# Optimization experiments

Hardware: AMD Instinct MI355X
Metric: run time of the kernel (lower is better)

The kernel has to match this reference:

```python
import jax, jax.numpy as jnp
import numpy as np

EPS = 1e-6

def _ln(x, g, b):
    m = x.mean(-1, keepdims=True)
    v = jnp.var(x, axis=-1, keepdims=True)
    return (x - m) * jax.lax.rsqrt(v + EPS) * g + b

def _mha(x, qkv_w, out_w, out_b, heads, dh):
    # vit-style attention: Linear(dim, 3*heads*dh, bias=False), chunk into q,k,v
    B, N, _ = x.shape
    qkv = (x @ qkv_w).reshape(B, N, 3, heads, dh).transpose(2, 0, 3, 1, 4)
    q, k, v = qkv[0], qkv[1], qkv[2]                       # [B,H,N,dh]
    attn = jax.nn.softmax(jnp.einsum('bhid,bhjd->bhij', q, k) * (dh ** -0.5), axis=-1)
    o = jnp.einsum('bhij,bhjd->bhid', attn, v).transpose(0, 2, 1, 3).reshape(B, N, heads * dh)
    return o @ out_w + out_b

def _tx(x, p, heads, dh):
    # standard prenorm transformer stack, p = stacked per-layer params
    (l1g, l1b, qw, ow, ob, l2g, l2b, f1w, f1b, f2w, f2b, ng, nb) = p
    for i in range(l1g.shape[0]):
        x = x + _mha(_ln(x, l1g[i], l1b[i]), qw[i], ow[i], ob[i], heads, dh)
        h = _ln(x, l2g[i], l2b[i])
        x = x + jax.nn.gelu(h @ f1w[i] + f1b[i]) @ f2w[i] + f2b[i]
    return _ln(x, ng, nb)

def _ats(x, l1g, l1b, qkvw, qkvb, projw, projb, l2g, l2b, f1w, f1b, f2w, f2b):
    # ATS block: attention + CLS-significance-driven adaptive token resampling (gather)
    B, N, D = x.shape
    heads = 6
    dh = D // heads
    h = _ln(x, l1g, l1b)
    qkv = (h @ qkvw + qkvb).reshape(B, N, 3, heads, dh).transpose(2, 0, 3, 1, 4)
    q, k, v = qkv[0], qkv[1], qkv[2]
    attn = jax.nn.softmax(jnp.einsum('bhid,bhjd->bhij', q, k) * (dh ** -0.5), axis=-1)  # [B,H,N,N]
    y = jnp.einsum('bhij,bhjd->bhid', attn, v).transpose(0, 2, 1, 3).reshape(B, N, D)
    y = y @ projw + projb
    # significance score: cls attention * value norm (ATS, Fayyaz et al.)
    vn = jnp.linalg.norm(v, axis=-1)                        # [B,H,N]
    s = (attn[:, :, 0, 1:] * vn[:, :, 1:]).mean(axis=1)     # [B,N-1]
    s = s / (s.sum(-1, keepdims=True) + 1e-8)
    cdf = jnp.cumsum(s, axis=-1)                            # [B,N-1]
    # deterministic inverse-transform sampling of N-1 tokens
    u = (jnp.arange(N - 1, dtype=x.dtype) + 0.5) / (N - 1)
    idx = jax.vmap(lambda c: jnp.searchsorted(c, u))(cdf)
    idx = jnp.clip(idx, 0, N - 2) + 1                       # skip cls slot
    idx = jnp.concatenate([jnp.zeros((B, 1), idx.dtype), idx], axis=1)  # keep cls
    g = lambda a: jnp.take_along_axis(a, idx[:, :, None], axis=1)
    x = g(x) + g(y)
    h = _ln(x, l2g, l2b)
    return x + jax.nn.gelu(h @ f1w + f1b) @ f2w + f2b

def reference(x, patch_w, patch_b, pos_emb, space_token, temporal_token,
              s_ln1_g, s_ln1_b, s_qkv_w, s_out_w, s_out_b, s_ln2_g, s_ln2_b,
              s_fc1_w, s_fc1_b, s_fc2_w, s_fc2_b, s_norm_g, s_norm_b,
              t_ln1_g, t_ln1_b, t_qkv_w, t_out_w, t_out_b, t_ln2_g, t_ln2_b,
              t_fc1_w, t_fc1_b, t_fc2_w, t_fc2_b, t_norm_g, t_norm_b,
              a_ln1_g, a_ln1_b, a_qkv_w, a_qkv_b, a_proj_w, a_proj_b,
              a_ln2_g, a_ln2_b, a_fc1_w, a_fc1_b, a_fc2_w, a_fc2_b,
              final_g, final_b, h1_w, h1_b, h2_w, h2_b):
    B, T = x.shape[0], x.shape[1]
    BT, D, P, HP = B * T, 192, 16, 14
    # patch embedding (conv16s16 as unfold + linear), channel-major flattening
    xt = x.reshape(BT, 3, HP, P, HP, P).transpose(0, 2, 4, 1, 3, 5).reshape(BT, HP * HP, 3 * P * P)
    xt = (xt @ patch_w + patch_b).reshape(B, T, HP * HP, D)
    cls = jnp.broadcast_to(space_token.reshape(1, 1, 1, D), (B, T, 1, D))
    xt = jnp.concatenate([cls, xt], axis=2) + pos_emb      # [B,T,197,D]
    xt = xt.reshape(BT, 197, D)
    xt = _tx(xt, (s_ln1_g, s_ln1_b, s_qkv_w, s_out_w, s_out_b, s_ln2_g, s_ln2_b,
                  s_fc1_w, s_fc1_b, s_fc2_w, s_fc2_b, s_norm_g, s_norm_b), 6, 64)
    for i in range(a_ln1_g.shape[0]):
        xt = _ats(xt, a_ln1_g[i], a_ln1_b[i], a_qkv_w[i], a_qkv_b[i], a_proj_w[i],
                  a_proj_b[i], a_ln2_g[i], a_ln2_b[i], a_fc1_w[i], a_fc1_b[i],
                  a_fc2_w[i], a_fc2_b[i])
    xc = xt[:, 0].reshape(B, T, D)
    tt = jnp.broadcast_to(temporal_token, (B, 1, D))
    xc = jnp.concatenate([tt, xc], axis=1)                 # [B,T+1,D]
    xc = _tx(xc, (t_ln1_g, t_ln1_b, t_qkv_w, t_out_w, t_out_b, t_ln2_g, t_ln2_b,
                  t_fc1_w, t_fc1_b, t_fc2_w, t_fc2_b, t_norm_g, t_norm_b), 6, 64)
    f = jnp.max(xc, axis=1)                                # AdaptiveMaxPool1d(1) over tokens
    f = _ln(f, final_g, final_b)
    return jax.nn.relu(f @ h1_w + h1_b) @ h2_w + h2_b      # mlp_head -> [B,2]

def setup_inputs():
    key = jax.random.key(0)
    ks = iter(jax.random.split(key, 64))
    def rn(shape, s=0.02):
        return jax.random.normal(next(ks), shape, dtype=jnp.float32) * s
    d = {}
    d['x'] = jax.random.normal(next(ks), (16, 5, 3, 224, 224), dtype=jnp.float32)
    d['patch_w'] = rn((768, 192)); d['patch_b'] = jnp.zeros((192,), jnp.float32)
    d['pos_emb'] = rn((1, 5, 197, 192))
    d['space_token'] = rn((1, 1, 192)); d['temporal_token'] = rn((1, 1, 192))
    def tx(depth, n):
        d[n + '_ln1_g'] = jnp.ones((depth, 192), jnp.float32); d[n + '_ln1_b'] = jnp.zeros((depth, 192), jnp.float32)
        d[n + '_qkv_w'] = rn((depth, 192, 1152)); d[n + '_out_w'] = rn((depth, 384, 192)); d[n + '_out_b'] = jnp.zeros((depth, 192), jnp.float32)
        d[n + '_ln2_g'] = jnp.ones((depth, 192), jnp.float32); d[n + '_ln2_b'] = jnp.zeros((depth, 192), jnp.float32)
        d[n + '_fc1_w'] = rn((depth, 192, 768)); d[n + '_fc1_b'] = jnp.zeros((depth, 768), jnp.float32)
        d[n + '_fc2_w'] = rn((depth, 768, 192)); d[n + '_fc2_b'] = jnp.zeros((depth, 192), jnp.float32)
        d[n + '_norm_g'] = jnp.ones((192,), jnp.float32); d[n + '_norm_b'] = jnp.zeros((192,), jnp.float32)
    tx(2, 's'); tx(3, 't')
    d['a_ln1_g'] = jnp.ones((12, 192), jnp.float32); d['a_ln1_b'] = jnp.zeros((12, 192), jnp.float32)
    d['a_qkv_w'] = rn((12, 192, 576)); d['a_qkv_b'] = jnp.zeros((12, 576), jnp.float32)
    d['a_proj_w'] = rn((12, 192, 192)); d['a_proj_b'] = jnp.zeros((12, 192), jnp.float32)
    d['a_ln2_g'] = jnp.ones((12, 192), jnp.float32); d['a_ln2_b'] = jnp.zeros((12, 192), jnp.float32)
    d['a_fc1_w'] = rn((12, 192, 768)); d['a_fc1_b'] = jnp.zeros((12, 768), jnp.float32)
    d['a_fc2_w'] = rn((12, 768, 192)); d['a_fc2_b'] = jnp.zeros((12, 192), jnp.float32)
    d['final_g'] = jnp.ones((192,), jnp.float32); d['final_b'] = jnp.zeros((192,), jnp.float32)
    d['h1_w'] = rn((192, 64)); d['h1_b'] = jnp.zeros((64,), jnp.float32)
    d['h2_w'] = rn((64, 2)); d['h2_b'] = jnp.zeros((2,), jnp.float32)
    return d
```

## Files before the change

kernel.cpp:

```cpp
#include <hip/hip_runtime.h>
#include <hip/hip_bf16.h>
#include <math.h>

typedef float in_t;
typedef float out_t;

__device__ __forceinline__ float ldi(const in_t* p, size_t i) { return (float)p[i]; }

#define DMODEL 192
#define NTOK   197
#define BT_    80
#define ROWS_  (BT_*NTOK)

__device__ __forceinline__ float gelu_f(float v) {
  return 0.5f*v*(1.f + tanhf(0.7978845608028654f*(v + 0.044715f*v*v*v)));
}

__device__ __forceinline__ short f2bf(float f) {
  union { float f; unsigned u; } v; v.f = f;
  unsigned r = v.u + 0x7FFFu + ((v.u >> 16) & 1u);
  return (short)(r >> 16);
}

typedef __attribute__((ext_vector_type(8))) short bfrag;
typedef __attribute__((ext_vector_type(4))) float f32x4;

__global__ __launch_bounds__(256)
void wconv_k(const float* __restrict__ W, short* __restrict__ O, int K, int N)
{
  __shared__ float tile[32][33];
  const int l = blockIdx.z;
  const int k0 = blockIdx.y*32, n0 = blockIdx.x*32;
  const float* Wl = W + (size_t)l*K*N;
  short* Ol = O + (size_t)l*K*N;
  const int tx = threadIdx.x & 31, ty = threadIdx.x >> 5;
  #pragma unroll
  for (int r = ty; r < 32; r += 8) {
    int k = k0 + r, n = n0 + tx;
    tile[r][tx] = (k < K && n < N) ? Wl[(size_t)k*N + n] : 0.f;
  }
  __syncthreads();
  #pragma unroll
  for (int r = ty; r < 32; r += 8) {
    int n = n0 + r, k = k0 + tx;
    if (n < N && k < K) Ol[(size_t)n*K + k] = f2bf(tile[tx][r]);
  }
}

template<int EPI>
__global__ __launch_bounds__(256)
void gemmM_k(const float* __restrict__ A, const short* __restrict__ Wt,
             const in_t* __restrict__ bias, const float* __restrict__ R,
             float* __restrict__ C, int M, int N, int K)
{
  constexpr int BM=64, BN=64, BK=32, LP=BK+8;
  __shared__ short Asb[BM][LP];
  __shared__ short Bsb[BN][LP];
  const int t = threadIdx.x;
  const int w = t >> 6, lane = t & 63;
  const int bm0 = blockIdx.y*BM, bn0 = blockIdx.x*BN;
  const int sr = t >> 2;
  const int sk = (t & 3) * 8;
  f32x4 acc[4] = {};

  for (int k0 = 0; k0 < K; k0 += BK) {
    {
      int gm = bm0 + sr;
      short y[8];
      if (gm < M) {
        const float* ap = A + (size_t)gm*K + k0 + sk;
        float4 v0 = *(const float4*)ap;
        float4 v1 = *(const float4*)(ap + 4);
        y[0]=f2bf(v0.x); y[1]=f2bf(v0.y); y[2]=f2bf(v0.z); y[3]=f2bf(v0.w);
        y[4]=f2bf(v1.x); y[5]=f2bf(v1.y); y[6]=f2bf(v1.z); y[7]=f2bf(v1.w);
      } else {
        #pragma unroll
        for (int i=0;i<8;++i) y[i]=0;
      }
      *(bfrag*)&Asb[sr][sk] = *(bfrag*)y;
      bfrag bv = *(const bfrag*)(Wt + (size_t)(bn0 + sr)*K + k0 + sk);
      *(bfrag*)&Bsb[sr][sk] = bv;
    }
    __syncthreads();
    const int fr = lane & 15, kg = (lane >> 4) * 8;
    bfrag af = *(const bfrag*)&Asb[w*16 + fr][kg];
    #pragma unroll
    for (int nt = 0; nt < 4; ++nt) {
      bfrag bf = *(const bfrag*)&Bsb[nt*16 + fr][kg];
      acc[nt] = __builtin_amdgcn_mfma_f32_16x16x32_bf16(af, bf, acc[nt], 0, 0, 0);
    }
    __syncthreads();
  }
  const int col = lane & 15, rg = (lane >> 4) * 4;
  #pragma unroll
  for (int nt = 0; nt < 4; ++nt) {
    int gn = bn0 + nt*16 + col;
    float bv = bias ? ldi(bias, gn) : 0.f;
    #pragma unroll
    for (int r = 0; r < 4; ++r) {
      int gm = bm0 + w*16 + rg + r;
      if (gm < M) {
        float v = acc[nt][r] + bv;
        if (EPI==1) v = gelu_f(v);
        if (EPI==2) v += R[(size_t)gm*N + gn];
        C[(size_t)gm*N + gn] = v;
      }
    }
  }
}

__global__ __launch_bounds__(256)
void ln_k(const float* __restrict__ x, const in_t* __restrict__ g, const in_t* __restrict__ b,
          float* __restrict__ o, int rows)
{
  int t = threadIdx.x, wave = t>>6, lane = t&63;
  int r = blockIdx.x*4 + wave;
  if (r >= rows) return;
  const float* xr = x + (size_t)r*DMODEL;
  float e0 = xr[lane], e1 = xr[lane+64], e2 = xr[lane+128];
  float s = e0+e1+e2;
  #pragma unroll
  for (int off=32; off; off>>=1) s += __shfl_xor(s, off);
  float mean = s / 192.f;
  float d0=e0-mean, d1=e1-mean, d2=e2-mean;
  float v = d0*d0+d1*d1+d2*d2;
  #pragma unroll
  for (int off=32; off; off>>=1) v += __shfl_xor(v, off);
  float rs = 1.f / sqrtf(v/192.f + 1e-6f);
  float* orow = o + (size_t)r*DMODEL;
  orow[lane]     = d0*rs*ldi(g,lane)     + ldi(b,lane);
  orow[lane+64]  = d1*rs*ldi(g,lane+64)  + ldi(b,lane+64);
  orow[lane+128] = d2*rs*ldi(g,lane+128) + ldi(b,lane+128);
}

template<int DH, int W>
__global__ __launch_bounds__(W*64)
void attnM_k(const float* __restrict__ qkv, float* __restrict__ out,
             float* __restrict__ attn0, int heads, float scale)
{
  constexpr int NSEQ = 197;
  constexpr int NP   = 224;
  constexpr int KG   = DH/8;
  constexpr int CT   = DH/16;
  constexpr int NF   = DH/32;
  __shared__ short Kb[KG][NP][8];
  __shared__ short Vt[NP/8][DH][8];
  __shared__ short Ps[W][NP/8][16][8];

  const int bh = blockIdx.x;
  const int b = bh / heads, h = bh - b*heads;
  const int stride = 3*heads*DH;
  const float* __restrict__ base = qkv + (size_t)b*NSEQ*stride;
  const int qo = h*DH, ko = heads*DH + h*DH, vo = 2*heads*DH + h*DH;
  const int t = threadIdx.x, w = t>>6, lane = t&63;

  for (int idx = t; idx < NP*DH; idx += W*64) {
    int j = idx / DH, d = idx - j*DH;
    float kv = 0.f, vv = 0.f;
    if (j < NSEQ) {
      kv = base[(size_t)j*stride + ko + d];
      vv = base[(size_t)j*stride + vo + d];
    }
    Kb[d>>3][j][d&7] = f2bf(kv);
    Vt[j>>3][d][j&7] = f2bf(vv);
  }
  __syncthreads();

  const int c = lane & 15, g = lane >> 4, rg = g*4;
  const float NEG = -3.0e38f;

  for (int st = w; st < 13; st += W) {
    const int q0 = st*16;
    int qrow = q0 + c; if (qrow > NSEQ-1) qrow = NSEQ-1;
    bfrag aq[NF];
    {
      const float* qp = base + (size_t)qrow*stride + qo + g*8;
      #pragma unroll
      for (int f = 0; f < NF; ++f) {
        float4 v0 = *(const float4*)(qp + f*32);
        float4 v1 = *(const float4*)(qp + f*32 + 4);
        short y[8] = {f2bf(v0.x),f2bf(v0.y),f2bf(v0.z),f2bf(v0.w),
                      f2bf(v1.x),f2bf(v1.y),f2bf(v1.z),f2bf(v1.w)};
        aq[f] = *(bfrag*)y;
      }
    }
    f32x4 sacc[14];
    #pragma unroll
    for (int jt = 0; jt < 14; ++jt) sacc[jt] = (f32x4){0.f,0.f,0.f,0.f};
    #pragma unroll
    for (int jt = 0; jt < 13; ++jt) {
      #pragma unroll
      for (int f = 0; f < NF; ++f) {
        bfrag bk = *(const bfrag*)&Kb[f*4 + g][jt*16 + c][0];
        sacc[jt] = __builtin_amdgcn_mfma_f32_16x16x32_bf16(aq[f], bk, sacc[jt], 0, 0, 0);
      }
    }
    float m0[4] = {NEG,NEG,NEG,NEG};
    #pragma unroll
    for (int jt = 0; jt < 14; ++jt) {
      const bool valid = (jt < 13) && (jt*16 + c < NSEQ);
      #pragma unroll
      for (int r = 0; r < 4; ++r) {
        float sv = valid ? sacc[jt][r]*scale : NEG;
        sacc[jt][r] = sv;
        m0[r] = fmaxf(m0[r], sv);
      }
    }
    #pragma unroll
    for (int off = 1; off < 16; off <<= 1)
      #pragma unroll
      for (int r = 0; r < 4; ++r) m0[r] = fmaxf(m0[r], __shfl_xor(m0[r], off));
    float sum[4] = {0.f,0.f,0.f,0.f};
    #pragma unroll
    for (int jt = 0; jt < 14; ++jt)
      #pragma unroll
      for (int r = 0; r < 4; ++r) {
        float e = expf(sacc[jt][r] - m0[r]);
        sacc[jt][r] = e;
        sum[r] += e;
      }
    #pragma unroll
    for (int off = 1; off < 16; off <<= 1)
      #pragma unroll
      for (int r = 0; r < 4; ++r) sum[r] += __shfl_xor(sum[r], off);
    float inv[4];
    #pragma unroll
    for (int r = 0; r < 4; ++r) inv[r] = 1.f / sum[r];

    if (attn0 != nullptr && st == 0 && g == 0) {
      #pragma unroll
      for (int jt = 0; jt < 13; ++jt) {
        int j = jt*16 + c;
        if (j < NSEQ) attn0[(size_t)bh*NSEQ + j] = sacc[jt][0]*inv[0];
      }
    }
    #pragma unroll
    for (int jt = 0; jt < 14; ++jt)
      #pragma unroll
      for (int r = 0; r < 4; ++r)
        Ps[w][jt*2 + (c>>3)][rg + r][c&7] = f2bf(sacc[jt][r]);
    f32x4 oacc[CT];
    #pragma unroll
    for (int ct = 0; ct < CT; ++ct) oacc[ct] = (f32x4){0.f,0.f,0.f,0.f};
    #pragma unroll
    for (int kc = 0; kc < 7; ++kc) {
      bfrag ap = *(const bfrag*)&Ps[w][kc*4 + g][c][0];
      #pragma unroll
      for (int ct = 0; ct < CT; ++ct) {
        bfrag bv = *(const bfrag*)&Vt[kc*4 + g][ct*16 + c][0];
        oacc[ct] = __builtin_amdgcn_mfma_f32_16x16x32_bf16(ap, bv, oacc[ct], 0, 0, 0);
      }
    }
    #pragma unroll
    for (int ct = 0; ct < CT; ++ct)
      #pragma unroll
      for (int r = 0; r < 4; ++r) {
        int q = q0 + rg + r;
        if (q < NSEQ)
          out[((size_t)b*NSEQ + q)*(size_t)(heads*DH) + h*DH + ct*16 + c] = oacc[ct][r]*inv[r];
      }
  }
}

template<int DH, int W>
__global__ __launch_bounds__(W*64)
void attn2r_k(const float* __restrict__ qkv, float* __restrict__ out,
              float* __restrict__ attn0, int Nseq, int heads, float scale)
{
  constexpr int QT = 8;
  constexpr int KTS = 204;
  constexpr int NPART = (DH == 64) ? 1 : 2;
  constexpr int DQ   = DH/4;
  constexpr int QPG  = 2;
  __shared__ float Kt[DH * KTS];
  __shared__ float Qt[W][DH][12];
  __shared__ float Ps[W][QT][200];

  const int bh = blockIdx.x;
  const int b = bh / heads, h = bh % heads;
  const int stride = 3 * heads * DH;
  const float* __restrict__ base = qkv + (size_t)b * Nseq * stride;
  const int qo = h * DH, ko = heads * DH + h * DH, vo = 2 * heads * DH + h * DH;
  const int t = threadIdx.x, w = t >> 6, lane = t & 63;

  for (int idx = t; idx < Nseq * DH; idx += W * 64) {
    int j = idx / DH, d0 = idx - j * DH;
    Kt[d0 * KTS + j] = base[(size_t)j * stride + ko + d0];
  }
  __syncthreads();

  const int d = lane & (DH - 1);
  const int nchunks = (Nseq + QT - 1) / QT;
  const int jcmax = (Nseq + 3) >> 2;
  const float NEG = -3.0e38f;
  const float4* Kt4 = (const float4*)Kt;

  const int part = (NPART == 2) ? (lane >> 5) : 0;
  const int qg   = (DH == 64) ? (lane >> 4) : ((lane >> 3) & 3);
  const int dq   = lane & (DQ - 1);
  const int dv   = 4 * dq;

  for (int ic = w; ic < nchunks; ic += W) {
    const int i0 = ic * QT;
    if ((DH == 64) || (lane >> 5) == 0) {
      #pragma unroll
      for (int q = 0; q < QT; ++q) {
        int i = i0 + q;
        Qt[w][d][q] = (i < Nseq) ? base[(size_t)i * stride + qo + d] : 0.f;
      }
    }
    float s[QT][4];
    #pragma unroll
    for (int q = 0; q < QT; ++q)
      #pragma unroll
      for (int u = 0; u < 4; ++u) s[q][u] = 0.f;
    #pragma unroll 4
    for (int dd = 0; dd < DH; ++dd) {
      float4 kv = (lane < 51) ? Kt4[dd * (KTS/4) + lane] : make_float4(0.f,0.f,0.f,0.f);
      float4 qA = *(const float4*)&Qt[w][dd][0];
      float4 qB = *(const float4*)&Qt[w][dd][4];
      float qv[8] = {qA.x, qA.y, qA.z, qA.w, qB.x, qB.y, qB.z, qB.w};
      float kr[4] = {kv.x, kv.y, kv.z, kv.w};
      #pragma unroll
      for (int q = 0; q < QT; ++q)
        #pragma unroll
        for (int u = 0; u < 4; ++u)
          s[q][u] = fmaf(qv[q], kr[u], s[q][u]);
    }
    float inv[QT];
    #pragma unroll
    for (int q = 0; q < QT; ++q) {
      float mx = NEG;
      #pragma unroll
      for (int u = 0; u < 4; ++u) {
        int j = 4*lane + u;
        s[q][u] = (j < Nseq) ? s[q][u]*scale : NEG;
        mx = fmaxf(mx, s[q][u]);
      }
      #pragma unroll
      for (int off = 32; off; off >>= 1) mx = fmaxf(mx, __shfl_xor(mx, off));
      float sum = 0.f;
      #pragma unroll
      for (int u = 0; u < 4; ++u) {
        float p = (4*lane + u < Nseq) ? expf(s[q][u] - mx) : 0.f;
        s[q][u] = p; sum += p;
      }
      #pragma unroll
      for (int off = 32; off; off >>= 1) sum += __shfl_xor(sum, off);
      inv[q] = 1.f / sum;
      if (lane < 50)
        *(float4*)&Ps[w][q][4*lane] = make_float4(s[q][0], s[q][1], s[q][2], s[q][3]);
    }
    if (attn0 != nullptr && i0 == 0) {
      #pragma unroll
      for (int u = 0; u < 4; ++u) {
        int j = 4*lane + u;
        if (j < Nseq) attn0[(size_t)bh*Nseq + j] = s[0][u]*inv[0];
      }
    }
    float o[QPG][4];
    #pragma unroll
    for (int qi = 0; qi < QPG; ++qi) { o[qi][0]=0.f; o[qi][1]=0.f; o[qi][2]=0.f; o[qi][3]=0.f; }
    const float* __restrict__ Vg = base + vo;
    for (int jc = part; jc < jcmax; jc += NPART) {
      const int jb = 4*jc;
      float4 V0 = make_float4(0.f,0.f,0.f,0.f), V1=V0, V2=V0, V3=V0;
      if (jb+0 < Nseq) V0 = *(const float4*)&Vg[(size_t)(jb+0)*stride + dv];
      if (jb+1 < Nseq) V1 = *(const float4*)&Vg[(size_t)(jb+1)*stride + dv];
      if (jb+2 < Nseq) V2 = *(const float4*)&Vg[(size_t)(jb+2)*stride + dv];
      if (jb+3 < Nseq) V3 = *(const float4*)&Vg[(size_t)(jb+3)*stride + dv];
      #pragma unroll
      for (int qi = 0; qi < QPG; ++qi) {
        float4 p4 = *(const float4*)&Ps[w][qg*QPG+qi][jb];
        o[qi][0] = fmaf(p4.w,V3.x, fmaf(p4.z,V2.x, fmaf(p4.y,V1.x, fmaf(p4.x,V0.x, o[qi][0]))));
        o[qi][1] = fmaf(p4.w,V3.y, fmaf(p4.z,V2.y, fmaf(p4.y,V1.y, fmaf(p4.x,V0.y, o[qi][1]))));
        o[qi][2] = fmaf(p4.w,V3.z, fmaf(p4.z,V2.z, fmaf(p4.y,V1.z, fmaf(p4.x,V0.z, o[qi][2]))));
        o[qi][3] = fmaf(p4.w,V3.w, fmaf(p4.z,V2.w, fmaf(p4.y,V1.w, fmaf(p4.x,V0.w, o[qi][3]))));
      }
    }
    if (NPART == 2) {
      #pragma unroll
      for (int qi = 0; qi < QPG; ++qi) {
        o[qi][0] += __shfl_xor(o[qi][0], 32);
        o[qi][1] += __shfl_xor(o[qi][1], 32);
        o[qi][2] += __shfl_xor(o[qi][2], 32);
        o[qi][3] += __shfl_xor(o[qi][3], 32);
      }
    }
    if (part == 0) {
      #pragma unroll
      for (int qi = 0; qi < QPG; ++qi) {
        float iv = inv[qi];
        if (qg == 1) iv = inv[QPG + qi];
        if (qg == 2) iv = inv[2*QPG + qi];
        if (qg == 3) iv = inv[3*QPG + qi];
        int i = i0 + qg*QPG + qi;
        if (i < Nseq) {
          float4 r = make_float4(o[qi][0]*iv, o[qi][1]*iv, o[qi][2]*iv, o[qi][3]*iv);
          *(float4*)&out[((size_t)b*Nseq + i)*(size_t)(heads*DH) + h*DH + dv] = r;
        }
      }
    }
  }
}

__global__ void patchify_k(const in_t* __restrict__ x, float* __restrict__ A)
{
  int idx = blockIdx.x*256 + threadIdx.x;
  const int total = BT_*196*768;
  if (idx >= total) return;
  int kc = idx % 768;
  int m  = idx / 768;
  int p  = m % 196;
  int bt = m / 196;
  int c  = kc >> 8;
  int py = (kc >> 4) & 15;
  int px = kc & 15;
  int ph = p / 14, pw = p % 14;
  size_t src = (((size_t)bt*3 + c)*224 + (ph*16+py))*224 + (pw*16+px);
  A[idx] = ldi(x, src);
}

__global__ void assemble_k(const float* __restrict__ pt, const in_t* __restrict__ st,
                           const in_t* __restrict__ pe, float* __restrict__ X)
{
  int i = blockIdx.x*256 + threadIdx.x;
  const int total = BT_*NTOK*DMODEL;
  if (i >= total) return;
  int d  = i % DMODEL;
  int n  = (i / DMODEL) % NTOK;
  int bt = i / (DMODEL*NTOK);
  int tt = bt % 5;
  float base = (n == 0) ? ldi(st, d)
                        : pt[((size_t)bt*196 + (n-1))*DMODEL + d];
  X[i] = base + ldi(pe, ((size_t)tt*NTOK + n)*DMODEL + d);
}

__global__ void score_k(const float* __restrict__ attn0, const float* __restrict__ qkv,
                        float* __restrict__ S)
{
  int b = blockIdx.x;
  int jj = threadIdx.x;
  if (jj >= 196) return;
  int j = jj + 1;
  float acc = 0.f;
  #pragma unroll
  for (int h = 0; h < 6; ++h) {
    float a0 = attn0[((size_t)b*6 + h)*NTOK + j];
    const float* v = qkv + ((size_t)b*NTOK + j)*576 + 384 + h*32;
    float ss = 0.f;
    #pragma unroll
    for (int d = 0; d < 32; ++d) ss += v[d]*v[d];
    acc += a0 * sqrtf(ss);
  }
  S[(size_t)b*196 + jj] = acc / 6.0f;
}

__global__ void sample_k(const float* __restrict__ S, int* __restrict__ idxout)
{
  __shared__ float cdf[196];
  int b = blockIdx.x, t = threadIdx.x;
  if (t == 0) {
    float tot = 0.f;
    for (int k = 0; k < 196; ++k) tot += S[(size_t)b*196 + k];
    float denom = tot + 1e-8f;
    float run = 0.f;
    for (int k = 0; k < 196; ++k) { run += S[(size_t)b*196 + k] / denom; cdf[k] = run; }
    idxout[(size_t)b*NTOK] = 0;
  }
  __syncthreads();
  if (t < 196) {
    float u = ((float)t + 0.5f) / 196.0f;
    int cnt = 0;
    for (int k = 0; k < 196; ++k) cnt += (cdf[k] < u) ? 1 : 0;
    int c = cnt > 195 ? 195 : cnt;
    idxout[(size_t)b*NTOK + 1 + t] = c + 1;
  }
}

__global__ void gather_k(const float* __restrict__ X, const float* __restrict__ P,
                         const int* __restrict__ idx, float* __restrict__ Xo)
{
  int i = blockIdx.x*256 + threadIdx.x;
  const int total = BT_*NTOK*DMODEL;
  if (i >= total) return;
  int d  = i % DMODEL;
  int n  = (i / DMODEL) % NTOK;
  int bt = i / (DMODEL*NTOK);
  int src = idx[(size_t)bt*NTOK + n];
  size_t sr = ((size_t)bt*NTOK + src)*DMODEL + d;
  Xo[i] = X[sr] + P[sr];
}

__global__ void build_xc_k(const float* __restrict__ X, const in_t* __restrict__ tt,
                           float* __restrict__ xc)
{
  int i = blockIdx.x*256 + threadIdx.x;
  const int total = 16*6*DMODEL;
  if (i >= total) return;
  int d = i % DMODEL;
  int n = (i / DMODEL) % 6;
  int b = i / (DMODEL*6);
  xc[i] = (n == 0) ? ldi(tt, d)
                   : X[(((size_t)b*5 + (n-1))*NTOK + 0)*DMODEL + d];
}

__global__ __launch_bounds__(256)
void head_k(const float* __restrict__ xc, const in_t* __restrict__ fg, const in_t* __restrict__ fb,
            const in_t* __restrict__ w1, const in_t* __restrict__ b1,
            const in_t* __restrict__ w2, const in_t* __restrict__ b2,
            out_t* __restrict__ outp)
{
  __shared__ float fn[DMODEL];
  __shared__ float hid[64];
  __shared__ float mv[2];
  int b = blockIdx.x, t = threadIdx.x;
  if (t < DMODEL) {
    float m = xc[((size_t)b*6 + 0)*DMODEL + t];
    #pragma unroll
    for (int n = 1; n < 6; ++n) m = fmaxf(m, xc[((size_t)b*6 + n)*DMODEL + t]);
    fn[t] = m;
  }
  __syncthreads();
  if (t == 0) {
    float s = 0.f;
    for (int d = 0; d < DMODEL; ++d) s += fn[d];
    float mean = s / 192.f;
    float v = 0.f;
    for (int d = 0; d < DMODEL; ++d) { float dd = fn[d]-mean; v += dd*dd; }
    mv[0] = mean; mv[1] = 1.f / sqrtf(v/192.f + 1e-6f);
  }
  __syncthreads();
  if (t < DMODEL) fn[t] = (fn[t]-mv[0])*mv[1]*ldi(fg,t) + ldi(fb,t);
  __syncthreads();
  if (t < 64) {
    float a = ldi(b1, t);
    for (int d = 0; d < DMODEL; ++d) a += fn[d]*ldi(w1, (size_t)d*64 + t);
    hid[t] = fmaxf(a, 0.f);
  }
  __syncthreads();
  if (t < 2) {
    float a = ldi(b2, t);
    for (int j = 0; j < 64; ++j) a += hid[j]*ldi(w2, (size_t)j*2 + t);
    outp[(size_t)b*2 + t] = (out_t)a;
  }
}

extern "C" void kernel_launch(void* const* d_in, const int* in_sizes, int n_in,
                              void* d_out, int out_size, void* d_ws, size_t ws_size,
                              hipStream_t stream)
{
  if (n_in < 50) return;
  const in_t* x_in     = (const in_t*)d_in[0];
  const in_t* patch_w  = (const in_t*)d_in[1];
  const in_t* patch_b  = (const in_t*)d_in[2];
  const in_t* pos_emb  = (const in_t*)d_in[3];
  const in_t* space_tk = (const in_t*)d_in[4];
  const in_t* temp_tk  = (const in_t*)d_in[5];
  const in_t* s_ln1_g = (const in_t*)d_in[6];  const in_t* s_ln1_b = (const in_t*)d_in[7];
  const in_t* s_qkv_w = (const in_t*)d_in[8];  const in_t* s_out_w = (const in_t*)d_in[9];
  const in_t* s_out_b = (const in_t*)d_in[10]; const in_t* s_ln2_g = (const in_t*)d_in[11];
  const in_t* s_ln2_b = (const in_t*)d_in[12]; const in_t* s_fc1_w = (const in_t*)d_in[13];
  const in_t* s_fc1_b = (const in_t*)d_in[14]; const in_t* s_fc2_w = (const in_t*)d_in[15];
  const in_t* s_fc2_b = (const in_t*)d_in[16]; const in_t* s_nrm_g = (const in_t*)d_in[17];
  const in_t* s_nrm_b = (const in_t*)d_in[18];
  const in_t* t_ln1_g = (const in_t*)d_in[19]; const in_t* t_ln1_b = (const in_t*)d_in[20];
  const in_t* t_qkv_w = (const in_t*)d_in[21]; const in_t* t_out_w = (const in_t*)d_in[22];
  const in_t* t_out_b = (const in_t*)d_in[23]; const in_t* t_ln2_g = (const in_t*)d_in[24];
  const in_t* t_ln2_b = (const in_t*)d_in[25]; const in_t* t_fc1_w = (const in_t*)d_in[26];
  const in_t* t_fc1_b = (const in_t*)d_in[27]; const in_t* t_fc2_w = (const in_t*)d_in[28];
  const in_t* t_fc2_b = (const in_t*)d_in[29]; const in_t* t_nrm_g = (const in_t*)d_in[30];
  const in_t* t_nrm_b = (const in_t*)d_in[31];
  const in_t* a_ln1_g = (const in_t*)d_in[32]; const in_t* a_ln1_b = (const in_t*)d_in[33];
  const in_t* a_qkv_w = (const in_t*)d_in[34]; const in_t* a_qkv_b = (const in_t*)d_in[35];
  const in_t* a_prj_w = (const in_t*)d_in[36]; const in_t* a_prj_b = (const in_t*)d_in[37];
  const in_t* a_ln2_g = (const in_t*)d_in[38]; const in_t* a_ln2_b = (const in_t*)d_in[39];
  const in_t* a_fc1_w = (const in_t*)d_in[40]; const in_t* a_fc1_b = (const in_t*)d_in[41];
  const in_t* a_fc2_w = (const in_t*)d_in[42]; const in_t* a_fc2_b = (const in_t*)d_in[43];
  const in_t* final_g = (const in_t*)d_in[44]; const in_t* final_b = (const in_t*)d_in[45];
  const in_t* h1_w = (const in_t*)d_in[46];    const in_t* h1_b = (const in_t*)d_in[47];
  const in_t* h2_w = (const in_t*)d_in[48];    const in_t* h2_b = (const in_t*)d_in[49];

  float* ws = (float*)d_ws;
  size_t off = 0;
  auto alloc = [&](size_t nf) { size_t r = off; off += (nf + 63) & ~((size_t)63); return r; };
  size_t oX   = alloc((size_t)ROWS_*DMODEL);
  size_t oX2  = alloc((size_t)ROWS_*DMODEL);
  size_t oH   = alloc((size_t)ROWS_*DMODEL);
  size_t oQKV = alloc((size_t)ROWS_*1152);
  size_t oY   = alloc((size_t)ROWS_*384);
  size_t oFF  = alloc((size_t)ROWS_*768);
  size_t oA0  = alloc((size_t)480*NTOK);
  size_t oSB  = alloc((size_t)BT_*196);
  size_t oXC  = alloc((size_t)16*6*DMODEL);
  size_t oIDX = alloc((size_t)BT_*NTOK);
  size_t oWB  = alloc((size_t)4202496 + 64);
  if (ws_size < off*sizeof(float)) return;

  float* X   = ws + oX;
  float* X2  = ws + oX2;
  float* H   = ws + oH;
  float* QKV = ws + oQKV;
  float* Y   = ws + oY;
  float* FF  = ws + oFF;
  float* A0  = ws + oA0;
  float* SB  = ws + oSB;
  float* XC  = ws + oXC;
  int*   IDX = (int*)(ws + oIDX);
  short* WB  = (short*)(ws + oWB);

  size_t wo = 0;
  auto wslot = [&](size_t n){ size_t r = wo; wo += n; return r; };
  size_t wPatch = wslot(147456);
  size_t wSqkv  = wslot(442368);
  size_t wSout  = wslot(147456);
  size_t wSfc1  = wslot(294912);
  size_t wSfc2  = wslot(294912);
  size_t wAqkv  = wslot(1327104);
  size_t wAprj  = wslot(442368);
  size_t wAfc1  = wslot(1769472);
  size_t wAfc2  = wslot(1769472);
  size_t wTqkv  = wslot(663552);
  size_t wTout  = wslot(221184);
  size_t wTfc1  = wslot(442368);
  size_t wTfc2  = wslot(442368);

  auto wconv = [&](const in_t* W, size_t slot, int K, int N, int L) {
    dim3 g(N/32, K/32, L);
    hipLaunchKernelGGL(wconv_k, g, dim3(256), 0, stream, W, WB + slot, K, N);
  };
  wconv(patch_w, wPatch, 768, 192, 1);
  wconv(s_qkv_w, wSqkv, 192, 1152, 2);
  wconv(s_out_w, wSout, 384, 192, 2);
  wconv(s_fc1_w, wSfc1, 192, 768, 2);
  wconv(s_fc2_w, wSfc2, 768, 192, 2);
  wconv(a_qkv_w, wAqkv, 192, 576, 12);
  wconv(a_prj_w, wAprj, 192, 192, 12);
  wconv(a_fc1_w, wAfc1, 192, 768, 12);
  wconv(a_fc2_w, wAfc2, 768, 192, 12);
  wconv(t_qkv_w, wTqkv, 192, 1152, 3);
  wconv(t_out_w, wTout, 384, 192, 3);
  wconv(t_fc1_w, wTfc1, 192, 768, 3);
  wconv(t_fc2_w, wTfc2, 768, 192, 3);

  auto gemm = [&](int epi, const float* A, const short* Wt, const in_t* bias,
                  const float* R, float* C, int M, int N, int K) {
    dim3 grid(N/64, (M+63)/64);
    if (epi == 0)      hipLaunchKernelGGL(gemmM_k<0>, grid, dim3(256), 0, stream, A, Wt, bias, R, C, M, N, K);
    else if (epi == 1) hipLaunchKernelGGL(gemmM_k<1>, grid, dim3(256), 0, stream, A, Wt, bias, R, C, M, N, K);
    else               hipLaunchKernelGGL(gemmM_k<2>, grid, dim3(256), 0, stream, A, Wt, bias, R, C, M, N, K);
  };
  auto ln = [&](const float* xi, const in_t* g, const in_t* b, float* o, int rows) {
    hipLaunchKernelGGL(ln_k, dim3((rows+3)/4), dim3(256), 0, stream, xi, g, b, o, rows);
  };

  {
    int total = BT_*196*768;
    hipLaunchKernelGGL(patchify_k, dim3((total+255)/256), dim3(256), 0, stream, x_in, FF);
    gemm(0, FF, WB + wPatch, patch_b, nullptr, Y, BT_*196, DMODEL, 768);
    int tot2 = BT_*NTOK*DMODEL;
    hipLaunchKernelGGL(assemble_k, dim3((tot2+255)/256), dim3(256), 0, stream, Y, space_tk, pos_emb, X);
  }

  const float sc64 = 0.125f;
  const float sc32 = 0.17677669529663687f;

  for (int i = 0; i < 2; ++i) {
    ln(X, s_ln1_g + (size_t)i*192, s_ln1_b + (size_t)i*192, H, ROWS_);
    gemm(0, H, WB + wSqkv + (size_t)i*192*1152, nullptr, nullptr, QKV, ROWS_, 1152, 192);
    hipLaunchKernelGGL((attnM_k<64,8>), dim3(BT_*6), dim3(512), 0, stream, QKV, Y, (float*)nullptr, 6, sc64);
    gemm(2, Y, WB + wSout + (size_t)i*384*192, s_out_b + (size_t)i*192, X, X, ROWS_, 192, 384);
    ln(X, s_ln2_g + (size_t)i*192, s_ln2_b + (size_t)i*192, H, ROWS_);
    gemm(1, H, WB + wSfc1 + (size_t)i*192*768, s_fc1_b + (size_t)i*768, nullptr, FF, ROWS_, 768, 192);
    gemm(2, FF, WB + wSfc2 + (size_t)i*768*192, s_fc2_b + (size_t)i*192, X, X, ROWS_, 192, 768);
  }
  ln(X, s_nrm_g, s_nrm_b, X, ROWS_);

  float* xa = X; float* xb = X2;
  for (int i = 0; i < 12; ++i) {
    ln(xa, a_ln1_g + (size_t)i*192, a_ln1_b + (size_t)i*192, H, ROWS_);
    gemm(0, H, WB + wAqkv + (size_t)i*192*576, a_qkv_b + (size_t)i*576, nullptr, QKV, ROWS_, 576, 192);
    hipLaunchKernelGGL((attnM_k<32,4>), dim3(BT_*6), dim3(256), 0, stream, QKV, Y, A0, 6, sc32);
    gemm(0, Y, WB + wAprj + (size_t)i*192*192, a_prj_b + (size_t)i*192, nullptr, H, ROWS_, 192, 192);
    hipLaunchKernelGGL(score_k, dim3(BT_), dim3(256), 0, stream, A0, QKV, SB);
    hipLaunchKernelGGL(sample_k, dim3(BT_), dim3(256), 0, stream, SB, IDX);
    {
      int tot = BT_*NTOK*DMODEL;
      hipLaunchKernelGGL(gather_k, dim3((tot+255)/256), dim3(256), 0, stream, xa, H, IDX, xb);
    }
    ln(xb, a_ln2_g + (size_t)i*192, a_ln2_b + (size_t)i*192, H, ROWS_);
    gemm(1, H, WB + wAfc1 + (size_t)i*192*768, a_fc1_b + (size_t)i*768, nullptr, FF, ROWS_, 768, 192);
    gemm(2, FF, WB + wAfc2 + (size_t)i*768*192, a_fc2_b + (size_t)i*192, xb, xb, ROWS_, 192, 768);
    float* tmp = xa; xa = xb; xb = tmp;
  }

  {
    int tot = 16*6*DMODEL;
    hipLaunchKernelGGL(build_xc_k, dim3((tot+255)/256), dim3(256), 0, stream, xa, temp_tk, XC);
  }
  const int MT = 16*6;
  for (int i = 0; i < 3; ++i) {
    ln(XC, t_ln1_g + (size_t)i*192, t_ln1_b + (size_t)i*192, H, MT);
    gemm(0, H, WB + wTqkv + (size_t)i*192*1152, nullptr, nullptr, QKV, MT, 1152, 192);
    hipLaunchKernelGGL((attn2r_k<64,8>), dim3(16*6), dim3(512), 0, stream, QKV, Y, (float*)nullptr, 6, 6, sc64);
    gemm(2, Y, WB + wTout + (size_t)i*384*192, t_out_b + (size_t)i*192, XC, XC, MT, 192, 384);
    ln(XC, t_ln2_g + (size_t)i*192, t_ln2_b + (size_t)i*192, H, MT);
    gemm(1, H, WB + wTfc1 + (size_t)i*192*768, t_fc1_b + (size_t)i*768, nullptr, FF, MT, 768, 192);
    gemm(2, FF, WB + wTfc2 + (size_t)i*768*192, t_fc2_b + (size_t)i*192, XC, XC, MT, 192, 768);
  }
  ln(XC, t_nrm_g, t_nrm_b, XC, MT);

  hipLaunchKernelGGL(head_k, dim3(16), dim3(256), 0, stream, XC, final_g, final_b,
                     h1_w, h1_b, h2_w, h2_b, (out_t*)d_out);
}
```

Measured before the change: 2.853 ms.

## Store GEMM intermediates in bf16 and deepen GEMM K-tile to 192

The GEMM kernel now stages a full 192-wide K chunk in LDS per iteration instead of 32, which cuts the number of barrier-synchronised load/compute rounds. It is also templated on bf16 input and output. Attention outputs, the GELU FFN hidden activations and the patchified input are now written as bf16, so the following GEMMs read half the bytes and skip the fp32-to-bf16 conversion. The larger LDS footprint (about 51 KB per block) may lower occupancy, and every K must now be a multiple of 192.

```diff
diff --git a/kernel.cpp b/kernel.cpp
--- a/kernel.cpp
+++ b/kernel.cpp
@@ -47,47 +47,53 @@
   }
 }
 
-template<int EPI>
+template<int EPI, int ABF, int OBF>
 __global__ __launch_bounds__(256)
-void gemmM_k(const float* __restrict__ A, const short* __restrict__ Wt,
-             const in_t* __restrict__ bias, const float* __restrict__ R,
-             float* __restrict__ C, int M, int N, int K)
-{
-  constexpr int BM=64, BN=64, BK=32, LP=BK+8;
-  __shared__ short Asb[BM][LP];
-  __shared__ short Bsb[BN][LP];
+void gemmW_k(const void* __restrict__ Ain, const short* __restrict__ Wt,
+             const float* __restrict__ bias, const float* __restrict__ R,
+             void* __restrict__ Cout, int M, int N, int K)
+{
+  constexpr int LP = 200;
+  __shared__ short Asb[64][LP];
+  __shared__ short Bsb[64][LP];
   const int t = threadIdx.x;
   const int w = t >> 6, lane = t & 63;
-  const int bm0 = blockIdx.y*BM, bn0 = blockIdx.x*BN;
+  const int bm0 = blockIdx.y*64, bn0 = blockIdx.x*64;
   const int sr = t >> 2;
   const int sk = (t & 3) * 8;
   f32x4 acc[4] = {};
 
-  for (int k0 = 0; k0 < K; k0 += BK) {
-    {
-      int gm = bm0 + sr;
-      short y[8];
+  for (int k0 = 0; k0 < K; k0 += 192) {
+    const int gm = bm0 + sr;
+    #pragma unroll
+    for (int cc = 0; cc < 6; ++cc) {
+      const int kk = cc*32 + sk;
+      short y[8] = {0,0,0,0,0,0,0,0};
       if (gm < M) {
-        const float* ap = A + (size_t)gm*K + k0 + sk;
-        float4 v0 = *(const float4*)ap;
-        float4 v1 = *(const float4*)(ap + 4);
-        y[0]=f2bf(v0.x); y[1]=f2bf(v0.y); y[2]=f2bf(v0.z); y[3]=f2bf(v0.w);
-        y[4]=f2bf(v1.x); y[5]=f2bf(v1.y); y[6]=f2bf(v1.z); y[7]=f2bf(v1.w);
-      } else {
-        #pragma unroll
-        for (int i=0;i<8;++i) y[i]=0;
-      }
-      *(bfrag*)&Asb[sr][sk] = *(bfrag*)y;
-      bfrag bv = *(const bfrag*)(Wt + (size_t)(bn0 + sr)*K + k0 + sk);
-      *(bfrag*)&Bsb[sr][sk] = bv;
+        if (ABF == 0) {
+          const float* ap = (const float*)Ain + (size_t)gm*K + k0 + kk;
+          float4 v0 = *(const float4*)ap;
+          float4 v1 = *(const float4*)(ap + 4);
+          y[0]=f2bf(v0.x); y[1]=f2bf(v0.y); y[2]=f2bf(v0.z); y[3]=f2bf(v0.w);
+          y[4]=f2bf(v1.x); y[5]=f2bf(v1.y); y[6]=f2bf(v1.z); y[7]=f2bf(v1.w);
+        } else {
+          *(bfrag*)y = *(const bfrag*)((const short*)Ain + (size_t)gm*K + k0 + kk);
+        }
+      }
+      *(bfrag*)&Asb[sr][kk] = *(bfrag*)y;
+      bfrag bv = *(const bfrag*)(Wt + (size_t)(bn0 + sr)*K + k0 + kk);
+      *(bfrag*)&Bsb[sr][kk] = bv;
     }
     __syncthreads();
-    const int fr = lane & 15, kg = (lane >> 4) * 8;
-    bfrag af = *(const bfrag*)&Asb[w*16 + fr][kg];
-    #pragma unroll
-    for (int nt = 0; nt < 4; ++nt) {
-      bfrag bf = *(const bfrag*)&Bsb[nt*16 + fr][kg];
-      acc[nt] = __builtin_amdgcn_mfma_f32_16x16x32_bf16(af, bf, acc[nt], 0, 0, 0);
+    const int fr = lane & 15, g8 = (lane >> 4) * 8;
+    #pragma unroll
+    for (int ks = 0; ks < 6; ++ks) {
+      bfrag af = *(const bfrag*)&Asb[w*16 + fr][ks*32 + g8];
+      #pragma unroll
+      for (int nt = 0; nt < 4; ++nt) {
+        bfrag bf = *(const bfrag*)&Bsb[nt*16 + fr][ks*32 + g8];
+        acc[nt] = __builtin_amdgcn_mfma_f32_16x16x32_bf16(af, bf, acc[nt], 0, 0, 0);
+      }
     }
     __syncthreads();
   }
@@ -95,7 +101,7 @@
   #pragma unroll
   for (int nt = 0; nt < 4; ++nt) {
     int gn = bn0 + nt*16 + col;
-    float bv = bias ? ldi(bias, gn) : 0.f;
+    float bv = bias ? bias[gn] : 0.f;
     #pragma unroll
     for (int r = 0; r < 4; ++r) {
       int gm = bm0 + w*16 + rg + r;
@@ -103,7 +109,8 @@
         float v = acc[nt][r] + bv;
         if (EPI==1) v = gelu_f(v);
         if (EPI==2) v += R[(size_t)gm*N + gn];
-        C[(size_t)gm*N + gn] = v;
+        if (OBF) ((short*)Cout)[(size_t)gm*N + gn] = f2bf(v);
+        else     ((float*)Cout)[(size_t)gm*N + gn] = v;
       }
     }
   }
@@ -135,7 +142,7 @@
 
 template<int DH, int W>
 __global__ __launch_bounds__(W*64)
-void attnM_k(const float* __restrict__ qkv, float* __restrict__ out,
+void attnM_k(const float* __restrict__ qkv, short* __restrict__ out,
              float* __restrict__ attn0, int heads, float scale)
 {
   constexpr int NSEQ = 197;
@@ -257,7 +264,7 @@
       for (int r = 0; r < 4; ++r) {
         int q = q0 + rg + r;
         if (q < NSEQ)
-          out[((size_t)b*NSEQ + q)*(size_t)(heads*DH) + h*DH + ct*16 + c] = oacc[ct][r]*inv[r];
+          out[((size_t)b*NSEQ + q)*(size_t)(heads*DH) + h*DH + ct*16 + c] = f2bf(oacc[ct][r]*inv[r]);
       }
   }
 }
@@ -404,7 +411,7 @@
   }
 }
 
-__global__ void patchify_k(const in_t* __restrict__ x, float* __restrict__ A)
+__global__ void patchify_k(const in_t* __restrict__ x, short* __restrict__ A)
 {
   int idx = blockIdx.x*256 + threadIdx.x;
   const int total = BT_*196*768;
@@ -418,7 +425,7 @@
   int px = kc & 15;
   int ph = p / 14, pw = p % 14;
   size_t src = (((size_t)bt*3 + c)*224 + (ph*16+py))*224 + (pw*16+px);
-  A[idx] = ldi(x, src);
+  A[idx] = f2bf(ldi(x, src));
 }
 
 __global__ void assemble_k(const float* __restrict__ pt, const in_t* __restrict__ st,
@@ -584,17 +591,19 @@
   float* ws = (float*)d_ws;
   size_t off = 0;
   auto alloc = [&](size_t nf) { size_t r = off; off += (nf + 63) & ~((size_t)63); return r; };
-  size_t oX   = alloc((size_t)ROWS_*DMODEL);
-  size_t oX2  = alloc((size_t)ROWS_*DMODEL);
-  size_t oH   = alloc((size_t)ROWS_*DMODEL);
-  size_t oQKV = alloc((size_t)ROWS_*1152);
-  size_t oY   = alloc((size_t)ROWS_*384);
-  size_t oFF  = alloc((size_t)ROWS_*768);
-  size_t oA0  = alloc((size_t)480*NTOK);
-  size_t oSB  = alloc((size_t)BT_*196);
-  size_t oXC  = alloc((size_t)16*6*DMODEL);
-  size_t oIDX = alloc((size_t)BT_*NTOK);
-  size_t oWB  = alloc((size_t)4202496 + 64);
+  size_t oX    = alloc((size_t)ROWS_*DMODEL);
+  size_t oX2   = alloc((size_t)ROWS_*DMODEL);
+  size_t oH    = alloc((size_t)ROWS_*DMODEL);
+  size_t oQKV  = alloc((size_t)ROWS_*1152);
+  size_t oY    = alloc((size_t)ROWS_*384);
+  size_t oA0   = alloc((size_t)480*NTOK);
+  size_t oSB   = alloc((size_t)BT_*196);
+  size_t oXC   = alloc((size_t)16*6*DMODEL);
+  size_t oIDX  = alloc((size_t)BT_*NTOK);
+  size_t oFFt  = alloc((size_t)96*768);
+  size_t oWB   = alloc((size_t)4202496 + 64);
+  size_t oYb   = alloc((size_t)ROWS_*384/2 + 64);
+  size_t oFFb  = alloc((size_t)ROWS_*768/2 + 64);
   if (ws_size < off*sizeof(float)) return;
 
   float* X   = ws + oX;
@@ -602,12 +611,14 @@
   float* H   = ws + oH;
   float* QKV = ws + oQKV;
   float* Y   = ws + oY;
-  float* FF  = ws + oFF;
   float* A0  = ws + oA0;
   float* SB  = ws + oSB;
   float* XC  = ws + oXC;
   int*   IDX = (int*)(ws + oIDX);
+  float* FFt = ws + oFFt;
   short* WB  = (short*)(ws + oWB);
+  short* Yb  = (short*)(ws + oYb);
+  short* FFb = (short*)(ws + oFFb);
 
   size_t wo = 0;
   auto wslot = [&](size_t n){ size_t r = wo; wo += n; return r; };
@@ -643,12 +654,15 @@
   wconv(t_fc1_w, wTfc1, 192, 768, 3);
   wconv(t_fc2_w, wTfc2, 768, 192, 3);
 
-  auto gemm = [&](int epi, const float* A, const short* Wt, const in_t* bias,
-                  const float* R, float* C, int M, int N, int K) {
+  auto gemm = [&](int epi, int abf, int obf, const void* A, const short* Wt,
+                  const float* bias, const float* R, void* C, int M, int N, int K) {
     dim3 grid(N/64, (M+63)/64);
-    if (epi == 0)      hipLaunchKernelGGL(gemmM_k<0>, grid, dim3(256), 0, stream, A, Wt, bias, R, C, M, N, K);
-    else if (epi == 1) hipLaunchKernelGGL(gemmM_k<1>, grid, dim3(256), 0, stream, A, Wt, bias, R, C, M, N, K);
-    else               hipLaunchKernelGGL(gemmM_k<2>, grid, dim3(256), 0, stream, A, Wt, bias, R, C, M, N, K);
+    if (epi==0 && abf==0)              hipLaunchKernelGGL((gemmW_k<0,0,0>), grid, dim3(256), 0, stream, A, Wt, bias, R, C, M, N, K);
+    else if (epi==0 && abf==1)         hipLaunchKernelGGL((gemmW_k<0,1,0>), grid, dim3(256), 0, stream, A, Wt, bias, R, C, M, N, K);
+    else if (epi==1 && obf==1)         hipLaunchKernelGGL((gemmW_k<1,0,1>), grid, dim3(256), 0, stream, A, Wt, bias, R, C, M, N, K);
+    else if (epi==1)                   hipLaunchKernelGGL((gemmW_k<1,0,0>), grid, dim3(256), 0, stream, A, Wt, bias, R, C, M, N, K);
+    else if (epi==2 && abf==1)         hipLaunchKernelGGL((gemmW_k<2,1,0>), grid, dim3(256), 0, stream, A, Wt, bias, R, C, M, N, K);
+    else                               hipLaunchKernelGGL((gemmW_k<2,0,0>), grid, dim3(256), 0, stream, A, Wt, bias, R, C, M, N, K);
   };
   auto ln = [&](const float* xi, const in_t* g, const in_t* b, float* o, int rows) {
     hipLaunchKernelGGL(ln_k, dim3((rows+3)/4), dim3(256), 0, stream, xi, g, b, o, rows);
@@ -656,8 +670,8 @@
 
   {
     int total = BT_*196*768;
-    hipLaunchKernelGGL(patchify_k, dim3((total+255)/256), dim3(256), 0, stream, x_in, FF);
-    gemm(0, FF, WB + wPatch, patch_b, nullptr, Y, BT_*196, DMODEL, 768);
+    hipLaunchKernelGGL(patchify_k, dim3((total+255)/256), dim3(256), 0, stream, x_in, FFb);
+    gemm(0, 1, 0, FFb, WB + wPatch, patch_b, nullptr, Y, 15680, 192, 768);
     int tot2 = BT_*NTOK*DMODEL;
     hipLaunchKernelGGL(assemble_k, dim3((tot2+255)/256), dim3(256), 0, stream, Y, space_tk, pos_emb, X);
   }
@@ -667,21 +681,21 @@
 
   for (int i = 0; i < 2; ++i) {
     ln(X, s_ln1_g + (size_t)i*192, s_ln1_b + (size_t)i*192, H, ROWS_);
-    gemm(0, H, WB + wSqkv + (size_t)i*192*1152, nullptr, nullptr, QKV, ROWS_, 1152, 192);
-    hipLaunchKernelGGL((attnM_k<64,8>), dim3(BT_*6), dim3(512), 0, stream, QKV, Y, (float*)nullptr, 6, sc64);
-    gemm(2, Y, WB + wSout + (size_t)i*384*192, s_out_b + (size_t)i*192, X, X, ROWS_, 192, 384);
+    gemm(0, 0, 0, H, WB + wSqkv + (size_t)i*192*1152, nullptr, nullptr, QKV, ROWS_, 1152, 192);
+    hipLaunchKernelGGL((attnM_k<64,8>), dim3(BT_*6), dim3(512), 0, stream, QKV, Yb, (float*)nullptr, 6, sc64);
+    gemm(2, 1, 0, Yb, WB + wSout + (size_t)i*384*192, s_out_b + (size_t)i*192, X, X, ROWS_, 192, 384);
     ln(X, s_ln2_g + (size_t)i*192, s_ln2_b + (size_t)i*192, H, ROWS_);
-    gemm(1, H, WB + wSfc1 + (size_t)i*192*768, s_fc1_b + (size_t)i*768, nullptr, FF, ROWS_, 768, 192);
-    gemm(2, FF, WB + wSfc2 + (size_t)i*768*192, s_fc2_b + (size_t)i*192, X, X, ROWS_, 192, 768);
+    gemm(1, 0, 1, H, WB + wSfc1 + (size_t)i*192*768, s_fc1_b + (size_t)i*768, nullptr, FFb, ROWS_, 768, 192);
+    gemm(2, 1, 0, FFb, WB + wSfc2 + (size_t)i*768*192, s_fc2_b + (size_t)i*192, X, X, ROWS_, 192, 768);
   }
   ln(X, s_nrm_g, s_nrm_b, X, ROWS_);
 
   float* xa = X; float* xb = X2;
   for (int i = 0; i < 12; ++i) {
     ln(xa, a_ln1_g + (size_t)i*192, a_ln1_b + (size_t)i*192, H, ROWS_);
-    gemm(0, H, WB + wAqkv + (size_t)i*192*576, a_qkv_b + (size_t)i*576, nullptr, QKV, ROWS_, 576, 192);
-    hipLaunchKernelGGL((attnM_k<32,4>), dim3(BT_*6), dim3(256), 0, stream, QKV, Y, A0, 6, sc32);
-    gemm(0, Y, WB + wAprj + (size_t)i*192*192, a_prj_b + (size_t)i*192, nullptr, H, ROWS_, 192, 192);
+    gemm(0, 0, 0, H, WB + wAqkv + (size_t)i*192*576, a_qkv_b + (size_t)i*576, nullptr, QKV, ROWS_, 576, 192);
+    hipLaunchKernelGGL((attnM_k<32,4>), dim3(BT_*6), dim3(256), 0, stream, QKV, Yb, A0, 6, sc32);
+    gemm(0, 1, 0, Yb, WB + wAprj + (size_t)i*192*192, a_prj_b + (size_t)i*192, nullptr, H, ROWS_, 192, 192);
     hipLaunchKernelGGL(score_k, dim3(BT_), dim3(256), 0, stream, A0, QKV, SB);
     hipLaunchKernelGGL(sample_k, dim3(BT_), dim3(256), 0, stream, SB, IDX);
     {
@@ -689,8 +703,8 @@
       hipLaunchKernelGGL(gather_k, dim3((tot+255)/256), dim3(256), 0, stream, xa, H, IDX, xb);
     }
     ln(xb, a_ln2_g + (size_t)i*192, a_ln2_b + (size_t)i*192, H, ROWS_);
-    gemm(1, H, WB + wAfc1 + (size_t)i*192*768, a_fc1_b + (size_t)i*768, nullptr, FF, ROWS_, 768, 192);
-    gemm(2, FF, WB + wAfc2 + (size_t)i*768*192, a_fc2_b + (size_t)i*192, xb, xb, ROWS_, 192, 768);
+    gemm(1, 0, 1, H, WB + wAfc1 + (size_t)i*192*768, a_fc1_b + (size_t)i*768, nullptr, FFb, ROWS_, 768, 192);
+    gemm(2, 1, 0, FFb, WB + wAfc2 + (size_t)i*768*192, a_fc2_b + (size_t)i*192, xb, xb, ROWS_, 192, 768);
     float* tmp = xa; xa = xb; xb = tmp;
   }
 
@@ -701,12 +715,12 @@
   const int MT = 16*6;
   for (int i = 0; i < 3; ++i) {
     ln(XC, t_ln1_g + (size_t)i*192, t_ln1_b + (size_t)i*192, H, MT);
-    gemm(0, H, WB + wTqkv + (size_t)i*192*1152, nullptr, nullptr, QKV, MT, 1152, 192);
+    gemm(0, 0, 0, H, WB + wTqkv + (size_t)i*192*1152, nullptr, nullptr, QKV, MT, 1152, 192);
     hipLaunchKernelGGL((attn2r_k<64,8>), dim3(16*6), dim3(512), 0, stream, QKV, Y, (float*)nullptr, 6, 6, sc64);
-    gemm(2, Y, WB + wTout + (size_t)i*384*192, t_out_b + (size_t)i*192, XC, XC, MT, 192, 384);
+    gemm(2, 0, 0, Y, WB + wTout + (size_t)i*384*192, t_out_b + (size_t)i*192, XC, XC, MT, 192, 384);
     ln(XC, t_ln2_g + (size_t)i*192, t_ln2_b + (size_t)i*192, H, MT);
-    gemm(1, H, WB + wTfc1 + (size_t)i*192*768, t_fc1_b + (size_t)i*768, nullptr, FF, MT, 768, 192);
-    gemm(2, FF, WB + wTfc2 + (size_t)i*768*192, t_fc2_b + (size_t)i*192, XC, XC, MT, 192, 768);
+    gemm(1, 0, 0, H, WB + wTfc1 + (size_t)i*192*768, t_fc1_b + (size_t)i*768, nullptr, FFt, MT, 768, 192);
+    gemm(2, 0, 0, FFt, WB + wTfc2 + (size_t)i*768*192, t_fc2_b + (size_t)i*192, XC, XC, MT, 192, 768);
   }
   ln(XC, t_nrm_g, t_nrm_b, XC, MT);
 
```

Result: no change. 2.830 ms (-0.8%).
